# Kernel tuning notes

Hardware: AMD Instinct MI355X
Metric: run time of the kernel (lower is better)

## Reference

```python
import jax, jax.numpy as jnp
import numpy as np

N_MICS = 8
MIC_RADIUS = 0.05
SAMPLE_RATE = 16000.0
SPEED_SOUND = 343.0
EPS = 1e-20
SPHERE_LEVELS = 4


def sphere_np(levels=SPHERE_LEVELS):
    # Faithful numpy port of the torch icosphere subdivision in sphere().
    h = 5.0 ** 0.5 / 5.0
    r = 2.0 / 5.0 * 5.0 ** 0.5
    pi = 3.141592654
    pts = np.zeros((12, 3), dtype=np.float32)
    pts[0] = [0.0, 0.0, 1.0]
    pts[11] = [0.0, 0.0, -1.0]
    k = np.arange(5, dtype=np.float32)
    pts[1:6, 0] = r * np.sin(2.0 * pi * k / 5.0)
    pts[1:6, 1] = r * np.cos(2.0 * pi * k / 5.0)
    pts[1:6, 2] = h
    pts[6:11, 0] = -r * np.sin(2.0 * pi * k / 5.0)
    pts[6:11, 1] = -r * np.cos(2.0 * pi * k / 5.0)
    pts[6:11, 2] = -h
    trs = np.array([[0, 2, 1], [0, 3, 2], [0, 4, 3], [0, 5, 4], [0, 1, 5],
                    [9, 1, 2], [10, 2, 3], [6, 3, 4], [7, 4, 5], [8, 5, 1],
                    [4, 7, 6], [5, 8, 7], [1, 9, 8], [2, 10, 9], [3, 6, 10],
                    [11, 6, 7], [11, 7, 8], [11, 8, 9], [11, 9, 10], [11, 10, 6]], dtype=np.int64)
    for _ in range(levels):
        T = trs.shape[0]
        sub = np.zeros((4 * T, 6), dtype=np.int64)
        sub[0 * T:1 * T] = trs[:, [0, 0, 0, 1, 2, 0]]
        sub[1 * T:2 * T] = trs[:, [0, 1, 1, 1, 1, 2]]
        sub[2 * T:3 * T] = trs[:, [2, 0, 1, 2, 2, 2]]
        sub[3 * T:4 * T] = trs[:, [0, 1, 1, 2, 2, 0]]
        flat = np.concatenate((sub[:, [0, 1]], sub[:, [2, 3]], sub[:, [4, 5]]), axis=0)
        srt = np.sort(flat, axis=1)
        m = srt.max()
        scal = srt[:, 0] * (m + 1) + srt[:, 1]
        uniq, inv = np.unique(scal, return_inverse=True)
        uv0 = uniq // (m + 1)
        uv1 = uniq - uv0 * (m + 1)
        trs = inv.reshape(3, -1).T
        pts = pts[uv0] + pts[uv1]
        pts /= np.sqrt((pts ** 2).sum(axis=1, keepdims=True))
    return pts.astype(np.float32)


def setup_inputs() -> dict:
    key = jax.random.key(0)
    # DOA grid and TDOAs from array geometry (precomputed in SrpPhat.__init__)
    doas_np = sphere_np()                                    # [2562, 3]
    ang = 2.0 * np.pi * np.arange(N_MICS) / N_MICS
    mics_np = np.stack([MIC_RADIUS * np.cos(ang), MIC_RADIUS * np.sin(ang),
                        np.zeros(N_MICS)], axis=1).astype(np.float32)  # [8, 3]
    taus_np = (SAMPLE_RATE / SPEED_SOUND) * (doas_np @ mics_np.T)      # [2562, 8]
    B, T, F, P = 4, 250, 513, N_MICS * (N_MICS + 1) // 2
    XXs = jax.random.normal(key, (B, T, F, 2, P), dtype=jnp.float32)
    return {"XXs": XXs, "taus": jnp.asarray(taus_np), "doas": jnp.asarray(doas_np)}


def reference(XXs, taus, doas):
    B, T, F, _, P = XXs.shape
    n_mics = taus.shape[1]
    D = taus.shape[0]
    frame_size = (F - 1) * 2
    # Steering phases: a = exp(-j * omega * tau)   [D, F, M]
    omegas = 2.0 * jnp.pi * jnp.arange(F, dtype=jnp.float32) / frame_size
    phase = omegas[None, :, None] * taus[:, None, :]
    A_re = jnp.cos(phase)
    A_im = -jnp.sin(phase)
    # Cross steering terms for every mic pair (triu incl. diagonal): W = a_i * conj(a_j)^H form
    i0, i1 = np.triu_indices(n_mics)                         # 36 pairs for 8 mics
    Ws_re = A_re[:, :, i0] * A_re[:, :, i1] + A_im[:, :, i0] * A_im[:, :, i1]  # [D, F, P]
    Ws_im = A_re[:, :, i0] * A_im[:, :, i1] - A_im[:, :, i0] * A_re[:, :, i1]
    # PHAT normalization of the cross-spectra
    XX_re = XXs[:, :, :, 0, :]
    XX_im = XXs[:, :, :, 1, :]
    mag = jnp.sqrt(XX_re ** 2 + XX_im ** 2) + EPS
    Xr = (XX_re / mag).reshape(B, T, F * P)
    Xi = (XX_im / mag).reshape(B, T, F * P)
    Wr = Ws_re.reshape(D, F * P)
    Wi = Ws_im.reshape(D, F * P)
    # SRP map: Re{ sum_fp XX_norm * conj(W) } reduced over freqs and pairs
    Ys = jnp.matmul(Xr, Wr.T) + jnp.matmul(Xi, Wi.T)         # [B, T, D]
    idx = jnp.argmax(Ys, axis=2)                             # [B, T]
    return doas[idx]                                         # [B, T, 3]
```

## Files before the change

### kernel.cpp

```cpp
#include <hip/hip_runtime.h>
#include <math.h>


#define F_BINS  513
#define M_TOTAL 1000
#define D_TOTAL 2562
#define D_PAD   2688
#define NPAIR   28
#define NC      32
#define K2      (NPAIR * NC)
#define S_SCALE 4.67f
#define NBT     4
#define FSPLIT  6
#define KSPB    2
#define KPS     448

#define OFF_COEF 0
#define OFF_TT   16512
#define OFF_G    (OFF_TT + (size_t)K2 * D_PAD)
#define OFF_GP   (OFF_G + (size_t)M_TOTAL * K2)
#define OFF_YS   OFF_GP

__device__ __constant__ int c_ptab[NPAIR] = {1,2,3,4,5,6,7, 9,10,11,12,13,14,
                                             16,17,18,19,20, 22,23,24,25,
                                             27,28,29, 31,32, 34};
__device__ __constant__ int c_i0[NPAIR] = {0,0,0,0,0,0,0, 1,1,1,1,1,1,
                                           2,2,2,2,2, 3,3,3,3, 4,4,4, 5,5, 6};
__device__ __constant__ int c_i1[NPAIR] = {1,2,3,4,5,6,7, 2,3,4,5,6,7,
                                           3,4,5,6,7, 4,5,6,7, 5,6,7, 6,7, 7};

__global__ void k_coef(float* __restrict__ coefEO) {
    __shared__ double sHC[NC][NC + 1];
    __shared__ double sHS[NC][NC + 1];
    const int f = blockIdx.x;
    const int t = threadIdx.x;
    const double z = (double)f * (M_PI / 512.0) * (double)S_SCALE;
    double th = M_PI * (t + 0.5) / NC;
    double ct = cos(th);
    double hs, hc;
    sincos(z * ct, &hs, &hc);
    double cp = 1.0, cc = ct, c2 = 2.0 * ct;
    sHC[0][t] = hc;      sHS[0][t] = hs;
    sHC[1][t] = hc * cc; sHS[1][t] = hs * cc;
    for (int n = 2; n < NC; ++n) {
        double cn = c2 * cc - cp;
        cp = cc; cc = cn;
        sHC[n][t] = hc * cn;
        sHS[n][t] = hs * cn;
    }
    __syncthreads();
    const int n = (t < 16) ? 2 * t : 2 * (t - 16) + 1;
    double sum = 0.0;
    if (t < 16) { for (int j = 0; j < NC; ++j) sum += sHC[n][j]; }
    else        { for (int j = 0; j < NC; ++j) sum += sHS[n][j]; }
    double scale = (n == 0) ? (1.0 / NC) : (2.0 / NC);
    coefEO[f * 32 + t] = (float)(sum * scale);
}

__global__ void k_ttab(const float* __restrict__ taus, float* __restrict__ Tt) {
    const int d = blockIdx.x * 256 + threadIdx.x;
    const int p = blockIdx.y;
    if (d >= D_PAD) return;
    const bool live = d < D_TOTAL;
    const int dd = live ? d : 0;
    const float u = (taus[dd * 8 + c_i0[p]] - taus[dd * 8 + c_i1[p]]) * (1.0f / S_SCALE);
    float* base = Tt + (size_t)p * 32 * D_PAD + d;
    base[0] = live ? 1.f : 0.f;
    base[(size_t)16 * D_PAD] = live ? u : 0.f;
    float tp = 1.f, tc = u;
    const float u2 = 2.f * u;
    for (int n = 2; n < NC; ++n) {
        float tn = u2 * tc - tp;
        tp = tc; tc = tn;
        int c = (n & 1) ? 16 + (n >> 1) : (n >> 1);
        base[(size_t)c * D_PAD] = live ? tn : 0.f;
    }
}

__global__ __launch_bounds__(256) void k_stageA(
    const float* __restrict__ XXs, const float* __restrict__ coefEO,
    float* __restrict__ Gp)
{
    __shared__ float sXn[16][NBT][64];
    __shared__ float sC[16][32];
    const int t     = threadIdx.x;
    const int bt0   = blockIdx.x * NBT;
    const int split = blockIdx.y;
    const int fbeg  = (F_BINS * split) / FSPLIT;
    const int fend  = (F_BINS * (split + 1)) / FSPLIT;
    const int p   = t & 31;
    const int sel = t >> 5;
    const bool im = sel >= 4;
    const int row = p + (im ? 32 : 0);
    const int c0  = (sel & 3) * 4 + (im ? 16 : 0);
    float acc[NBT][4] = {};

    for (int fc = fbeg; fc < fend; fc += 16) {
        const int cnt = min(16, fend - fc);
        __syncthreads();
        for (int e = t; e < cnt * 8; e += 256)
            *(float4*)&sC[0][e * 4] = *(const float4*)&coefEO[fc * 32 + e * 4];
        for (int e = t; e < NBT * cnt * 28; e += 256) {
            int pp   = e % 28;
            int rest = e / 28;
            int fl   = rest % cnt;
            int bt   = rest / cnt;
            const float* bp = XXs + ((size_t)(bt0 + bt) * F_BINS + (fc + fl)) * 72;
            int po = c_ptab[pp];
            float xr = bp[po];
            float xi = bp[36 + po];
            float inv = 1.f / (sqrtf(xr * xr + xi * xi) + 1e-20f);
            sXn[fl][bt][pp]      = xr * inv;
            sXn[fl][bt][32 + pp] = xi * inv;
        }
        __syncthreads();
        for (int fl = 0; fl < cnt; ++fl) {
            float4 c4 = *(const float4*)&sC[fl][c0];
            #pragma unroll
            for (int bt = 0; bt < NBT; ++bt) {
                float a = sXn[fl][bt][row];
                acc[bt][0] = fmaf(a, c4.x, acc[bt][0]);
                acc[bt][1] = fmaf(a, c4.y, acc[bt][1]);
                acc[bt][2] = fmaf(a, c4.z, acc[bt][2]);
                acc[bt][3] = fmaf(a, c4.w, acc[bt][3]);
            }
        }
    }
    if (p < NPAIR) {
        float* gsp = Gp + (size_t)split * M_TOTAL * K2;
        #pragma unroll
        for (int bt = 0; bt < NBT; ++bt) {
            float4 v = {acc[bt][0], acc[bt][1], acc[bt][2], acc[bt][3]};
            *(float4*)&gsp[(size_t)(bt0 + bt) * K2 + p * 32 + c0] = v;
        }
    }
}

__global__ void k_reduceG(const float* __restrict__ Gp, float* __restrict__ G) {
    const int i = blockIdx.x * 256 + threadIdx.x;
    const size_t MK = (size_t)M_TOTAL * K2;
    if (i < (int)MK) {
        float s = 0.f;
        #pragma unroll
        for (int k = 0; k < FSPLIT; ++k) s += Gp[i + k * MK];
        G[i] = s;
    }
}

#define BKB 32
__global__ __launch_bounds__(256) void k_gemmB(
    const float* __restrict__ G, const float* __restrict__ Tt,
    float* __restrict__ Ysp)
{
    __shared__ float sAT[64][33];
    __shared__ float sB[BKB][132];
    const int t = threadIdx.x;
    const int row0 = blockIdx.x * 64;
    const int col0 = blockIdx.y * 128;
    const int koff = blockIdx.z * KPS;
    const int tx = t & 15;
    const int ty = t >> 4;
    float acc[4][8] = {};

    for (int k0 = 0; k0 < KPS; k0 += BKB) {
        __syncthreads();
        for (int e = t; e < 64 * BKB; e += 256) {
            int r = e >> 5, kk = e & 31;
            int rg = row0 + r;
            sAT[r][kk] = (rg < M_TOTAL) ? G[(size_t)rg * K2 + koff + k0 + kk] : 0.f;
        }
        for (int e = t; e < 1024; e += 256) {
            int kk = e >> 5, cq = e & 31;
            *(float4*)&sB[kk][cq * 4] =
                *(const float4*)&Tt[(size_t)(koff + k0 + kk) * D_PAD + col0 + cq * 4];
        }
        __syncthreads();
        #pragma unroll 8
        for (int kk = 0; kk < BKB; ++kk) {
            float av[4];
            #pragma unroll
            for (int i = 0; i < 4; ++i) av[i] = sAT[ty * 4 + i][kk];
            float4 b0 = *(const float4*)&sB[kk][tx * 8];
            float4 b1 = *(const float4*)&sB[kk][tx * 8 + 4];
            float bv[8] = {b0.x, b0.y, b0.z, b0.w, b1.x, b1.y, b1.z, b1.w};
            #pragma unroll
            for (int i = 0; i < 4; ++i)
                #pragma unroll
                for (int j = 0; j < 8; ++j)
                    acc[i][j] = fmaf(av[i], bv[j], acc[i][j]);
        }
    }
    float* yp = Ysp + (size_t)blockIdx.z * M_TOTAL * D_PAD;
    #pragma unroll
    for (int i = 0; i < 4; ++i) {
        int rg = row0 + ty * 4 + i;
        if (rg >= M_TOTAL) continue;
        float* y = yp + (size_t)rg * D_PAD + col0 + tx * 8;
        float4 v0 = {acc[i][0], acc[i][1], acc[i][2], acc[i][3]};
        float4 v1 = {acc[i][4], acc[i][5], acc[i][6], acc[i][7]};
        *(float4*)&y[0] = v0;
        *(float4*)&y[4] = v1;
    }
}

__global__ __launch_bounds__(256) void k_argmax(
    const float* __restrict__ Ysp, const float* __restrict__ doas,
    float* __restrict__ out)
{
    __shared__ float sv[256];
    __shared__ int   si[256];
    const int row = blockIdx.x;
    const int tid = threadIdx.x;
    const float* y0 = Ysp + (size_t)row * D_PAD;
    const float* y1 = y0 + (size_t)M_TOTAL * D_PAD;
    float best = -INFINITY;
    int bi = D_TOTAL;
    for (int d = tid; d < D_TOTAL; d += 256) {
        float v = y0[d] + y1[d];
        if (v > best) { best = v; bi = d; }
    }
    sv[tid] = best; si[tid] = bi;
    __syncthreads();
    for (int s = 128; s > 0; s >>= 1) {
        if (tid < s) {
            float v2 = sv[tid + s]; int i2 = si[tid + s];
            if (v2 > sv[tid] || (v2 == sv[tid] && i2 < si[tid])) { sv[tid] = v2; si[tid] = i2; }
        }
        __syncthreads();
    }
    if (tid == 0) {
        int idx = si[0];
        out[row * 3 + 0] = doas[idx * 3 + 0];
        out[row * 3 + 1] = doas[idx * 3 + 1];
        out[row * 3 + 2] = doas[idx * 3 + 2];
    }
}

extern "C" void kernel_launch(void* const* d_in, const int* in_sizes, int n_in,
                              void* d_out, int out_size, void* d_ws, size_t ws_size,
                              hipStream_t stream) {
    const float* XXs  = (const float*)d_in[0];
    const float* taus = (const float*)d_in[1];
    const float* doas = (const float*)d_in[2];
    float* ws     = (float*)d_ws;
    float* coefEO = ws + OFF_COEF;
    float* Tt     = ws + OFF_TT;
    float* G      = ws + OFF_G;
    float* Gp     = ws + OFF_GP;
    float* Ysp    = ws + OFF_YS;

    k_coef   <<<F_BINS, 32, 0, stream>>>(coefEO);
    k_ttab   <<<dim3((D_PAD + 255) / 256, NPAIR), 256, 0, stream>>>(taus, Tt);
    k_stageA <<<dim3(M_TOTAL / NBT, FSPLIT), 256, 0, stream>>>(XXs, coefEO, Gp);
    k_reduceG<<<(M_TOTAL * K2 + 255) / 256, 256, 0, stream>>>(Gp, G);
    k_gemmB  <<<dim3(16, D_PAD / 128, KSPB), 256, 0, stream>>>(G, Tt, Ysp);
    k_argmax <<<M_TOTAL, 256, 0, stream>>>(Ysp, doas, (float*)d_out);
}
```

Baseline: 387.7 us.

## Prefetch XXs with vector loads in stageA and transpose G for GEMM

Stage A now loads the cross-spectra with float4 vector loads, double-buffering the next frequency chunk in registers while it computes the current one. It uses 128-thread blocks with 8 outputs per thread and keeps the whole split's coefficients resident in shared memory. The G reduction now writes a transposed, padded Gt so the GEMM can load A tiles with coalesced float4 reads, and the GEMM tile is reshaped to 128x64. The aim is to cut strided scalar global loads and hide memory latency, at the cost of higher register pressure and extra loads of unused diagonal pair entries.

```diff
diff --git a/kernel.cpp b/kernel.cpp
--- a/kernel.cpp
+++ b/kernel.cpp
@@ -11,14 +11,16 @@
 #define K2      (NPAIR * NC)
 #define S_SCALE 4.67f
 #define NBT     4
+#define CNT     8
 #define FSPLIT  6
 #define KSPB    2
 #define KPS     448
+#define BT_PAD  1024
 
 #define OFF_COEF 0
 #define OFF_TT   16512
-#define OFF_G    (OFF_TT + (size_t)K2 * D_PAD)
-#define OFF_GP   (OFF_G + (size_t)M_TOTAL * K2)
+#define OFF_GT   (OFF_TT + (size_t)K2 * D_PAD)
+#define OFF_GP   (OFF_GT + (size_t)K2 * BT_PAD)
 #define OFF_YS   OFF_GP
 
 __device__ __constant__ int c_ptab[NPAIR] = {1,2,3,4,5,6,7, 9,10,11,12,13,14,
@@ -28,6 +30,15 @@
                                            2,2,2,2,2, 3,3,3,3, 4,4,4, 5,5, 6};
 __device__ __constant__ int c_i1[NPAIR] = {1,2,3,4,5,6,7, 2,3,4,5,6,7,
                                            3,4,5,6,7, 4,5,6,7, 5,6,7, 6,7, 7};
+__device__ __constant__ int c_inv[36] = {
+    -1, 0, 1, 2, 3, 4, 5, 6,
+    -1, 7, 8, 9,10,11,12,
+    -1,13,14,15,16,17,
+    -1,18,19,20,21,
+    -1,22,23,24,
+    -1,25,26,
+    -1,27,
+    -1};
 
 __global__ void k_coef(float* __restrict__ coefEO) {
     __shared__ double sHC[NC][NC + 1];
@@ -77,129 +88,191 @@
     }
 }
 
-__global__ __launch_bounds__(256) void k_stageA(
+#define NSLOT 3
+__global__ __launch_bounds__(128, 3) void k_stageA(
     const float* __restrict__ XXs, const float* __restrict__ coefEO,
     float* __restrict__ Gp)
 {
-    __shared__ float sXn[16][NBT][64];
-    __shared__ float sC[16][32];
+    __shared__ float4 sXn4[NBT][CNT / 4][64];
+    __shared__ float  sCall[88][32];
     const int t     = threadIdx.x;
     const int bt0   = blockIdx.x * NBT;
     const int split = blockIdx.y;
     const int fbeg  = (F_BINS * split) / FSPLIT;
     const int fend  = (F_BINS * (split + 1)) / FSPLIT;
+    const int nf    = fend - fbeg;
     const int p   = t & 31;
     const int sel = t >> 5;
-    const bool im = sel >= 4;
-    const int row = p + (im ? 32 : 0);
-    const int c0  = (sel & 3) * 4 + (im ? 16 : 0);
-    float acc[NBT][4] = {};
-
-    for (int fc = fbeg; fc < fend; fc += 16) {
-        const int cnt = min(16, fend - fc);
-        __syncthreads();
-        for (int e = t; e < cnt * 8; e += 256)
-            *(float4*)&sC[0][e * 4] = *(const float4*)&coefEO[fc * 32 + e * 4];
-        for (int e = t; e < NBT * cnt * 28; e += 256) {
-            int pp   = e % 28;
-            int rest = e / 28;
-            int fl   = rest % cnt;
-            int bt   = rest / cnt;
-            const float* bp = XXs + ((size_t)(bt0 + bt) * F_BINS + (fc + fl)) * 72;
-            int po = c_ptab[pp];
-            float xr = bp[po];
-            float xi = bp[36 + po];
-            float inv = 1.f / (sqrtf(xr * xr + xi * xi) + 1e-20f);
-            sXn[fl][bt][pp]      = xr * inv;
-            sXn[fl][bt][32 + pp] = xi * inv;
-        }
-        __syncthreads();
-        for (int fl = 0; fl < cnt; ++fl) {
-            float4 c4 = *(const float4*)&sC[fl][c0];
+    const bool im = sel >= 2;
+    const int row = (p < NPAIR ? p : NPAIR - 1) + (im ? 32 : 0);
+    const int c0  = (sel & 1) * 8 + (im ? 16 : 0);
+
+    for (int e = t; e < 88 * 8; e += 128) {
+        int fl = e >> 3, q = e & 7;
+        int f  = fbeg + fl; if (f > F_BINS - 1) f = F_BINS - 1;
+        *(float4*)&sCall[fl][q * 4] = *(const float4*)&coefEO[f * 32 + q * 4];
+    }
+
+    float acc[NBT][8] = {};
+    float4 cur_re[NSLOT], cur_im[NSLOT], nxt_re[NSLOT], nxt_im[NSLOT];
+
+    auto issue = [&](int fc, float4* vre, float4* vim) {
+        const int cnt = min(CNT, fend - fc);
+        #pragma unroll
+        for (int s = 0; s < NSLOT; ++s) {
+            int e = t + s * 128;
+            float4 z4 = {0.f, 0.f, 0.f, 0.f};
+            vre[s] = z4; vim[s] = z4;
+            if (e < NBT * CNT * 9) {
+                int q   = e % 9;
+                int rbf = e / 9;
+                int bt  = rbf / CNT;
+                int fl  = rbf - bt * CNT;
+                if (fl < cnt) {
+                    const float* bp = XXs + (((size_t)(bt0 + bt) * F_BINS) + fc + fl) * 72;
+                    vre[s] = *(const float4*)&bp[q * 4];
+                    vim[s] = *(const float4*)&bp[36 + q * 4];
+                }
+            }
+        }
+    };
+
+    issue(fbeg, cur_re, cur_im);
+
+    for (int fc = fbeg; fc < fend; fc += CNT) {
+        __syncthreads();
+        #pragma unroll
+        for (int s = 0; s < NSLOT; ++s) {
+            int e = t + s * 128;
+            if (e >= NBT * CNT * 9) break;
+            int q   = e % 9;
+            int rbf = e / 9;
+            int bt  = rbf / CNT;
+            int fl  = rbf - bt * CNT;
+            float* dst = (float*)&sXn4[bt][fl >> 2][0];
+            const float* xr4 = (const float*)&cur_re[s];
+            const float* xi4 = (const float*)&cur_im[s];
+            #pragma unroll
+            for (int j = 0; j < 4; ++j) {
+                int pp = c_inv[q * 4 + j];
+                if (pp >= 0) {
+                    float xr = xr4[j], xi = xi4[j];
+                    float inv = 1.f / (sqrtf(xr * xr + xi * xi) + 1e-20f);
+                    dst[pp * 4 + (fl & 3)]        = xr * inv;
+                    dst[(32 + pp) * 4 + (fl & 3)] = xi * inv;
+                }
+            }
+        }
+        if (fc + CNT < fend) issue(fc + CNT, nxt_re, nxt_im);
+        __syncthreads();
+        const int cbase = fc - fbeg;
+        #pragma unroll
+        for (int fg = 0; fg < CNT / 4; ++fg) {
+            float4 cjA[4], cjB[4];
+            #pragma unroll
+            for (int j = 0; j < 4; ++j) {
+                cjA[j] = *(const float4*)&sCall[cbase + fg * 4 + j][c0];
+                cjB[j] = *(const float4*)&sCall[cbase + fg * 4 + j][c0 + 4];
+            }
             #pragma unroll
             for (int bt = 0; bt < NBT; ++bt) {
-                float a = sXn[fl][bt][row];
-                acc[bt][0] = fmaf(a, c4.x, acc[bt][0]);
-                acc[bt][1] = fmaf(a, c4.y, acc[bt][1]);
-                acc[bt][2] = fmaf(a, c4.z, acc[bt][2]);
-                acc[bt][3] = fmaf(a, c4.w, acc[bt][3]);
+                float4 a4 = sXn4[bt][fg][row];
+                float av[4] = {a4.x, a4.y, a4.z, a4.w};
+                #pragma unroll
+                for (int j = 0; j < 4; ++j) {
+                    acc[bt][0] = fmaf(av[j], cjA[j].x, acc[bt][0]);
+                    acc[bt][1] = fmaf(av[j], cjA[j].y, acc[bt][1]);
+                    acc[bt][2] = fmaf(av[j], cjA[j].z, acc[bt][2]);
+                    acc[bt][3] = fmaf(av[j], cjA[j].w, acc[bt][3]);
+                    acc[bt][4] = fmaf(av[j], cjB[j].x, acc[bt][4]);
+                    acc[bt][5] = fmaf(av[j], cjB[j].y, acc[bt][5]);
+                    acc[bt][6] = fmaf(av[j], cjB[j].z, acc[bt][6]);
+                    acc[bt][7] = fmaf(av[j], cjB[j].w, acc[bt][7]);
+                }
             }
         }
-    }
+        #pragma unroll
+        for (int s = 0; s < NSLOT; ++s) { cur_re[s] = nxt_re[s]; cur_im[s] = nxt_im[s]; }
+    }
+
     if (p < NPAIR) {
         float* gsp = Gp + (size_t)split * M_TOTAL * K2;
         #pragma unroll
         for (int bt = 0; bt < NBT; ++bt) {
-            float4 v = {acc[bt][0], acc[bt][1], acc[bt][2], acc[bt][3]};
-            *(float4*)&gsp[(size_t)(bt0 + bt) * K2 + p * 32 + c0] = v;
-        }
-    }
-}
-
-__global__ void k_reduceG(const float* __restrict__ Gp, float* __restrict__ G) {
+            float* g = gsp + (size_t)(bt0 + bt) * K2 + p * 32 + c0;
+            float4 v0 = {acc[bt][0], acc[bt][1], acc[bt][2], acc[bt][3]};
+            float4 v1 = {acc[bt][4], acc[bt][5], acc[bt][6], acc[bt][7]};
+            *(float4*)&g[0] = v0;
+            *(float4*)&g[4] = v1;
+        }
+    }
+}
+
+__global__ void k_reduceG(const float* __restrict__ Gp, float* __restrict__ Gt) {
     const int i = blockIdx.x * 256 + threadIdx.x;
     const size_t MK = (size_t)M_TOTAL * K2;
     if (i < (int)MK) {
+        int bt = i / K2, k = i - bt * K2;
         float s = 0.f;
         #pragma unroll
-        for (int k = 0; k < FSPLIT; ++k) s += Gp[i + k * MK];
-        G[i] = s;
+        for (int pl = 0; pl < FSPLIT; ++pl) s += Gp[i + pl * MK];
+        Gt[(size_t)k * BT_PAD + bt] = s;
+    } else if (i < K2 * BT_PAD) {
+        int j = i - (int)MK;
+        int btp = j / K2, k = j - btp * K2;
+        Gt[(size_t)k * BT_PAD + M_TOTAL + btp] = 0.f;
     }
 }
 
 #define BKB 32
-__global__ __launch_bounds__(256) void k_gemmB(
-    const float* __restrict__ G, const float* __restrict__ Tt,
+__global__ __launch_bounds__(256, 4) void k_gemmB(
+    const float* __restrict__ Gt, const float* __restrict__ Tt,
     float* __restrict__ Ysp)
 {
-    __shared__ float sAT[64][33];
-    __shared__ float sB[BKB][132];
+    __shared__ float sA[BKB][136];
+    __shared__ float sB[BKB][68];
     const int t = threadIdx.x;
-    const int row0 = blockIdx.x * 64;
-    const int col0 = blockIdx.y * 128;
+    const int row0 = blockIdx.x * 128;
+    const int col0 = blockIdx.y * 64;
     const int koff = blockIdx.z * KPS;
     const int tx = t & 15;
     const int ty = t >> 4;
-    float acc[4][8] = {};
+    float acc[8][4] = {};
 
     for (int k0 = 0; k0 < KPS; k0 += BKB) {
         __syncthreads();
-        for (int e = t; e < 64 * BKB; e += 256) {
-            int r = e >> 5, kk = e & 31;
-            int rg = row0 + r;
-            sAT[r][kk] = (rg < M_TOTAL) ? G[(size_t)rg * K2 + koff + k0 + kk] : 0.f;
-        }
         for (int e = t; e < 1024; e += 256) {
-            int kk = e >> 5, cq = e & 31;
-            *(float4*)&sB[kk][cq * 4] =
-                *(const float4*)&Tt[(size_t)(koff + k0 + kk) * D_PAD + col0 + cq * 4];
+            int kk = e >> 5, r4 = (e & 31) * 4;
+            *(float4*)&sA[kk][r4] =
+                *(const float4*)&Gt[(size_t)(koff + k0 + kk) * BT_PAD + row0 + r4];
+        }
+        for (int e = t; e < 512; e += 256) {
+            int kk = e >> 4, c4 = (e & 15) * 4;
+            *(float4*)&sB[kk][c4] =
+                *(const float4*)&Tt[(size_t)(koff + k0 + kk) * D_PAD + col0 + c4];
         }
         __syncthreads();
         #pragma unroll 8
         for (int kk = 0; kk < BKB; ++kk) {
-            float av[4];
+            float4 a0 = *(const float4*)&sA[kk][ty * 8];
+            float4 a1 = *(const float4*)&sA[kk][ty * 8 + 4];
+            float4 b  = *(const float4*)&sB[kk][tx * 4];
+            float av[8] = {a0.x, a0.y, a0.z, a0.w, a1.x, a1.y, a1.z, a1.w};
+            float bv[4] = {b.x, b.y, b.z, b.w};
             #pragma unroll
-            for (int i = 0; i < 4; ++i) av[i] = sAT[ty * 4 + i][kk];
-            float4 b0 = *(const float4*)&sB[kk][tx * 8];
-            float4 b1 = *(const float4*)&sB[kk][tx * 8 + 4];
-            float bv[8] = {b0.x, b0.y, b0.z, b0.w, b1.x, b1.y, b1.z, b1.w};
-            #pragma unroll
-            for (int i = 0; i < 4; ++i)
+            for (int i = 0; i < 8; ++i)
                 #pragma unroll
-                for (int j = 0; j < 8; ++j)
+                for (int j = 0; j < 4; ++j)
                     acc[i][j] = fmaf(av[i], bv[j], acc[i][j]);
         }
     }
     float* yp = Ysp + (size_t)blockIdx.z * M_TOTAL * D_PAD;
     #pragma unroll
-    for (int i = 0; i < 4; ++i) {
-        int rg = row0 + ty * 4 + i;
+    for (int i = 0; i < 8; ++i) {
+        int rg = row0 + ty * 8 + i;
         if (rg >= M_TOTAL) continue;
-        float* y = yp + (size_t)rg * D_PAD + col0 + tx * 8;
-        float4 v0 = {acc[i][0], acc[i][1], acc[i][2], acc[i][3]};
-        float4 v1 = {acc[i][4], acc[i][5], acc[i][6], acc[i][7]};
-        *(float4*)&y[0] = v0;
-        *(float4*)&y[4] = v1;
+        float4 v = {acc[i][0], acc[i][1], acc[i][2], acc[i][3]};
+        *(float4*)(yp + (size_t)rg * D_PAD + col0 + tx * 4) = v;
     }
 }
 
@@ -245,14 +318,14 @@
     float* ws     = (float*)d_ws;
     float* coefEO = ws + OFF_COEF;
     float* Tt     = ws + OFF_TT;
-    float* G      = ws + OFF_G;
+    float* Gt     = ws + OFF_GT;
     float* Gp     = ws + OFF_GP;
     float* Ysp    = ws + OFF_YS;
 
     k_coef   <<<F_BINS, 32, 0, stream>>>(coefEO);
     k_ttab   <<<dim3((D_PAD + 255) / 256, NPAIR), 256, 0, stream>>>(taus, Tt);
-    k_stageA <<<dim3(M_TOTAL / NBT, FSPLIT), 256, 0, stream>>>(XXs, coefEO, Gp);
-    k_reduceG<<<(M_TOTAL * K2 + 255) / 256, 256, 0, stream>>>(Gp, G);
-    k_gemmB  <<<dim3(16, D_PAD / 128, KSPB), 256, 0, stream>>>(G, Tt, Ysp);
+    k_stageA <<<dim3(M_TOTAL / NBT, FSPLIT), 128, 0, stream>>>(XXs, coefEO, Gp);
+    k_reduceG<<<(K2 * BT_PAD + 255) / 256, 256, 0, stream>>>(Gp, Gt);
+    k_gemmB  <<<dim3(BT_PAD / 128, D_PAD / 64, KSPB), 256, 0, stream>>>(Gt, Tt, Ysp);
     k_argmax <<<M_TOTAL, 256, 0, stream>>>(Ysp, doas, (float*)d_out);
 }
```

Result: faster. 341.6 us (-11.9%).
